# Optimization experiments

Hardware: AMD Instinct MI355X
Metric: run time of the kernel (lower is better)

Reference implementation:

```python
import jax, jax.numpy as jnp
from jax import lax
import numpy as np

B, N, C = 4, 2000, 80           # images, proposals/img, foreground classes
SCORE_THR = 0.05
IOU_THR = 0.5
MAX_PER_IMG = 100
K_PRE = 2000                     # pre-NMS top-k candidates per image
STDS = np.array([0.1, 0.1, 0.2, 0.2], dtype=np.float32)
MAX_RATIO = float(abs(np.log(16.0 / 1000.0)))  # wh_ratio_clip=16/1000


def setup_inputs() -> dict:
    key = jax.random.key(0)
    k1, k2, k3 = jax.random.split(key, 3)
    class_outs = jax.random.normal(k1, (B, N, C + 1), dtype=jnp.float32)
    regression_outs = jax.random.normal(k2, (B, N, C * 4), dtype=jnp.float32) * 0.5
    # random valid proposal boxes inside 800x1333 images (x1<x2, y1<y2)
    xy = jax.random.uniform(k3, (B, N, 2, 2), dtype=jnp.float32)
    xy = xy * jnp.array([1333.0, 800.0], dtype=jnp.float32)
    lo = jnp.min(xy, axis=2)
    hi = jnp.max(xy, axis=2) + 1.0
    boxes = jnp.concatenate([lo, hi], axis=-1)  # [B,N,4] x1,y1,x2,y2
    images_hw = jnp.tile(jnp.array([[800, 1333]], dtype=jnp.int32), (B, 1))
    return {"class_outs": class_outs, "regression_outs": regression_outs,
            "boxes": boxes, "images_hw": images_hw}


def _decode(props, deltas, h, w):
    # props [N,4], deltas [N,C,4] -> decoded boxes [N,C,4], clipped to image
    d = deltas * jnp.asarray(STDS)
    dx, dy, dw, dh = d[..., 0], d[..., 1], d[..., 2], d[..., 3]
    dw = jnp.clip(dw, -MAX_RATIO, MAX_RATIO)
    dh = jnp.clip(dh, -MAX_RATIO, MAX_RATIO)
    px = (props[:, None, 0] + props[:, None, 2]) * 0.5
    py = (props[:, None, 1] + props[:, None, 3]) * 0.5
    pw = props[:, None, 2] - props[:, None, 0]
    ph = props[:, None, 3] - props[:, None, 1]
    gx = px + pw * dx
    gy = py + ph * dy
    gw = pw * jnp.exp(dw)
    gh = ph * jnp.exp(dh)
    x1 = jnp.clip(gx - gw * 0.5, 0.0, w)
    y1 = jnp.clip(gy - gh * 0.5, 0.0, h)
    x2 = jnp.clip(gx + gw * 0.5, 0.0, w)
    y2 = jnp.clip(gy + gh * 0.5, 0.0, h)
    return jnp.stack([x1, y1, x2, y2], axis=-1)


def _pairwise_iou(b):
    # b [K,4] -> iou [K,K]
    area = (b[:, 2] - b[:, 0]) * (b[:, 3] - b[:, 1])
    lt = jnp.maximum(b[:, None, :2], b[None, :, :2])
    rb = jnp.minimum(b[:, None, 2:], b[None, :, 2:])
    wh = jnp.clip(rb - lt, 0.0)
    inter = wh[..., 0] * wh[..., 1]
    return inter / (area[:, None] + area[None, :] - inter + 1e-6)


def _process_image(cls_out, reg_out, props, hw):
    h = hw[0].astype(jnp.float32)
    w = hw[1].astype(jnp.float32)
    scores = jax.nn.softmax(cls_out, axis=-1)[:, :C]          # drop background col
    bboxes = _decode(props, reg_out.reshape(N, C, 4), h, w)   # [N,C,4]
    flat_scores = scores.reshape(-1)                          # [N*C]
    flat_boxes = bboxes.reshape(-1, 4)
    labels = jnp.tile(jnp.arange(C, dtype=jnp.int32), N)      # class fastest-varying
    cand = jnp.where(flat_scores > SCORE_THR, flat_scores, -1.0)
    top_scores, top_idx = lax.top_k(cand, K_PRE)
    top_boxes = flat_boxes[top_idx]
    top_labels = labels[top_idx]
    valid = top_scores > SCORE_THR
    # class-offset trick: boxes of distinct classes never overlap
    off = top_labels.astype(jnp.float32)[:, None] * (jnp.maximum(h, w) + 1.0)
    iou = _pairwise_iou(top_boxes + off)                      # [K_PRE,K_PRE]
    idxs = jnp.arange(K_PRE)

    def body(i, keep):
        sup = (idxs > i) & (iou[i] > IOU_THR) & keep[i]
        return keep & ~sup

    keep = lax.fori_loop(0, K_PRE, body, valid)
    kept_scores = jnp.where(keep, top_scores, -1.0)
    det_scores, det_i = lax.top_k(kept_scores, MAX_PER_IMG)
    det_valid = det_scores > SCORE_THR
    det_boxes = jnp.where(det_valid[:, None], top_boxes[det_i], 0.0)
    det_labels = jnp.where(det_valid, top_labels[det_i], -1)
    det_scores = jnp.where(det_valid, det_scores, 0.0)
    return det_boxes, det_scores, det_labels


def reference(class_outs, regression_outs, boxes, images_hw):
    det_boxes, det_scores, det_labels = jax.vmap(_process_image)(
        class_outs, regression_outs, boxes, images_hw)
    return det_boxes, det_scores, det_labels
```

## Files before the change

### kernel.cpp

```cpp
#include <hip/hip_runtime.h>


typedef unsigned long long u64;
typedef unsigned int u32;

#define B_ 4
#define N_ 2000
#define C_ 80
#define NCLS 81
#define KPRE 2000
#define MAXDET 100
#define TARGET 192
#define NB 2312
#define NBPAD 2368
#define NG 37
#define HBASE 0xF500
#define KSHIFT 46
#define CAPA 256
#define CAPB 2048
#define CAPIMG 8192
#define KPT 8
#define BPI 125
#define BIGI 0x7fffffff
#define MAXR 4.135166556742356f

#define WS_GCUR  0
#define WS_GHIST 64
#define WS_GFLAG 37952
#define WS_GKEYS 38016
#define WS_GBOX  300160
#define WS_ZEND  37952

__device__ __forceinline__ u64 pack_key(float score, unsigned fi) {
  return ((u64)__float_as_uint(score) << 32) | (u64)(0xFFFFFFFFu - fi);
}
__device__ __forceinline__ int bucket_of_bits(u32 sb) {
  return min(max((int)(sb >> 14) - HBASE, 0), NB - 1);
}
__device__ __forceinline__ u64 rdlane64(u64 v, int l) {
  u32 lo = (u32)__builtin_amdgcn_readlane((int)(u32)v, l);
  u32 hi = (u32)__builtin_amdgcn_readlane((int)(v >> 32), l);
  return ((u64)hi << 32) | lo;
}

__device__ __forceinline__ float wred_max(float v) {
  int t;
#define STEPM(ctrl)                                                          \
  t = __builtin_amdgcn_update_dpp(__float_as_int(v), __float_as_int(v),      \
                                  (ctrl), 0xF, 0xF, false);                  \
  v = fmaxf(v, __int_as_float(t));
  STEPM(0x111) STEPM(0x112) STEPM(0x114) STEPM(0x118) STEPM(0x142) STEPM(0x143)
#undef STEPM
  return __int_as_float(__builtin_amdgcn_readlane(__float_as_int(v), 63));
}
__device__ __forceinline__ float wred_sum(float v) {
  int t;
#define STEPS(ctrl)                                                          \
  t = __builtin_amdgcn_update_dpp(0, __float_as_int(v), (ctrl), 0xF, 0xF,    \
                                  false);                                    \
  v = v + __int_as_float(t);
  STEPS(0x111) STEPS(0x112) STEPS(0x114) STEPS(0x118) STEPS(0x142) STEPS(0x143)
#undef STEPS
  return __int_as_float(__builtin_amdgcn_readlane(__float_as_int(v), 63));
}

__device__ __forceinline__ float4 decode_one(
    u64 kk, const float* __restrict__ reg, const float* __restrict__ props,
    int b, float h, float w, float offscale) {
  unsigned fi = 0xFFFFFFFFu - (u32)kk;
  int n = (int)(fi / (unsigned)C_);
  int c = (int)(fi - (unsigned)n * (unsigned)C_);
  float4 p = ((const float4*)props)[b * N_ + n];
  const float* dl = reg + ((size_t)(b * N_ + n)) * (C_ * 4) + c * 4;
  float dx = dl[0] * 0.1f;
  float dy = dl[1] * 0.1f;
  float dw = fminf(fmaxf(dl[2] * 0.2f, -MAXR), MAXR);
  float dh = fminf(fmaxf(dl[3] * 0.2f, -MAXR), MAXR);
  float px = (p.x + p.z) * 0.5f, py = (p.y + p.w) * 0.5f;
  float pw = p.z - p.x, ph = p.w - p.y;
  float gx = px + pw * dx, gy = py + ph * dy;
  float gw = pw * expf(dw), gh = ph * expf(dh);
  float off = (float)c * offscale;
  return make_float4(fminf(fmaxf(gx - gw * 0.5f, 0.0f), w) + off,
                     fminf(fmaxf(gy - gh * 0.5f, 0.0f), h) + off,
                     fminf(fmaxf(gx + gw * 0.5f, 0.0f), w) + off,
                     fminf(fmaxf(gy + gh * 0.5f, 0.0f), h) + off);
}

__global__ __launch_bounds__(1024) void cand_kernel(
    const float* __restrict__ cls, const float* __restrict__ reg,
    const float* __restrict__ props, const int* __restrict__ hw,
    u64* __restrict__ gkeys, float4* __restrict__ gbox,
    u32* __restrict__ gcur, u32* __restrict__ ghist) {
  __shared__ int s_wc[16], s_woff[16];
  __shared__ int s_base;
  const int tid = threadIdx.x;
  const int wvi = tid >> 6, lane = tid & 63;
  const int blk = blockIdx.x;
  const int b = blk / BPI;
  const int n = (blk % BPI) * 16 + wvi;
  const float* lg = cls + (size_t)(b * N_ + n) * NCLS;
  float x0 = lg[lane];
  float x1 = (lane < 17) ? lg[64 + lane] : -3.0e38f;
  float mx = wred_max(fmaxf(x0, x1));
  float e0 = expf(x0 - mx);
  float e1 = (lane < 17) ? expf(x1 - mx) : 0.0f;
  float sum = wred_sum(e0 + e1);
  float sc0 = e0 / sum, sc1 = e1 / sum;
  bool p0 = sc0 > 0.05f;
  bool p1 = (lane < 16) && (sc1 > 0.05f);
  u64 m0 = __ballot(p0), m1 = __ballot(p1);
  int c0 = __popcll(m0);
  if (lane == 0) s_wc[wvi] = c0 + __popcll(m1);
  __syncthreads();
  if (tid == 0) {
    int acc = 0;
#pragma unroll
    for (int i = 0; i < 16; ++i) { s_woff[i] = acc; acc += s_wc[i]; }
    s_base = (acc > 0) ? (int)atomicAdd(&gcur[b], (u32)acc) : 0;
  }
  __syncthreads();
  const int base = s_base + s_woff[wvi];
  const u64 lt = (1ull << lane) - 1;
  u64* gk = gkeys + (size_t)b * CAPIMG;
  float4* gbx = gbox + (size_t)b * CAPIMG;
  u32* gh = ghist + (size_t)b * NBPAD;
  float hh = (float)hw[b * 2 + 0];
  float ww = (float)hw[b * 2 + 1];
  float offscale = fmaxf(hh, ww) + 1.0f;
  float4 p = ((const float4*)props)[b * N_ + n];
  float px = (p.x + p.z) * 0.5f, py = (p.y + p.w) * 0.5f;
  float pw = p.z - p.x, ph = p.w - p.y;
#pragma unroll 1
  for (int t = 0; t < 2; t++) {
    bool pp = t ? p1 : p0;
    if (!pp) continue;
    float sc = t ? sc1 : sc0;
    int c = t ? (64 + lane) : lane;
    int slot = base + (t ? (c0 + __popcll(m1 & lt)) : __popcll(m0 & lt));
    atomicAdd(&gh[bucket_of_bits(__float_as_uint(sc))], 1u);
    if (slot < CAPIMG) {
      gk[slot] = pack_key(sc, (unsigned)(n * C_ + c));
      const float4 d4 =
          *(const float4*)(reg + ((size_t)(b * N_ + n)) * (C_ * 4) + c * 4);
      float dx = d4.x * 0.1f, dy = d4.y * 0.1f;
      float dw = fminf(fmaxf(d4.z * 0.2f, -MAXR), MAXR);
      float dh = fminf(fmaxf(d4.w * 0.2f, -MAXR), MAXR);
      float gx = px + pw * dx, gy = py + ph * dy;
      float gw = pw * expf(dw), gh2 = ph * expf(dh);
      float off = (float)c * offscale;
      gbx[slot] = make_float4(fminf(fmaxf(gx - gw * 0.5f, 0.0f), ww) + off,
                              fminf(fmaxf(gy - gh2 * 0.5f, 0.0f), hh) + off,
                              fminf(fmaxf(gx + gw * 0.5f, 0.0f), ww) + off,
                              fminf(fmaxf(gy + gh2 * 0.5f, 0.0f), hh) + off);
    }
  }
}

__global__ __launch_bounds__(1024) void nms_kernel(
    const int* __restrict__ hw, const u64* __restrict__ gkeys,
    const float4* __restrict__ gbox, const u32* __restrict__ gcur,
    const u32* __restrict__ ghist, int* __restrict__ gflag,
    float* __restrict__ out) {
  __shared__ u64 lds8[3596];
  char* bp = (char*)lds8;
  u64* U = (u64*)bp;
  u64* SS = (u64*)(bp + 2080);
  u64* rb = (u64*)(bp + 4128);
  float4* bxA = (float4*)(bp + 12320);
  u32* s_hist = (u32*)(bp + 16416);
  u32* Upos = (u32*)(bp + 25888);
  int* rankA = (int*)(bp + 26912);
  int* outl = (int*)(bp + 27936);
  int* s_coarse = (int*)(bp + 28448);
  int* misc = (int*)(bp + 28704);

  const int b = blockIdx.x, tid = threadIdx.x;
  const int wv = tid >> 6, lane = tid & 63;

  if (tid < 16 && tid != 5 && tid != 7) misc[tid] = 0;
  if (tid >= NG && tid < 64) s_coarse[tid] = 0;
  if (tid == 512) {
    u32 Mraw = gcur[b];
    misc[5] = min((int)Mraw, CAPIMG);
    misc[7] = (Mraw > (u32)CAPIMG) ? 1 : 0;
  }

  for (int g2 = wv; g2 < NG; g2 += 16) {
    int v = (int)ghist[b * NBPAD + ((g2 << 6) | lane)];
    s_hist[(g2 << 6) | lane] = (u32)v;
#pragma unroll
    for (int o = 32; o; o >>= 1) v += __shfl_xor(v, o);
    if (lane == 0) s_coarse[g2] = v;
  }
  __syncthreads();

  if (tid < 64) {
    int v = s_coarse[lane];
#pragma unroll
    for (int off = 1; off < 64; off <<= 1) {
      int src = lane + off;
      int o = __shfl(v, src < 64 ? src : 63);
      if (src < 64) v += o;
    }
    int Mtot = __shfl(v, 0);
    u64 pm = __ballot(v >= TARGET);
    int T_A = 0, S_A;
    if (pm) {
      int gs = 63 - __builtin_clzll(pm);
      int beyond = __shfl(v, gs + 1);
      int fv = (int)s_hist[(gs << 6) | lane];
#pragma unroll
      for (int off = 1; off < 64; off <<= 1) {
        int src = lane + off;
        int o = __shfl(fv, src < 64 ? src : 63);
        if (src < 64) fv += o;
      }
      int cum = beyond + fv;
      u64 pm2 = __ballot(cum >= TARGET);
      int tr = 63 - __builtin_clzll(pm2);
      T_A = (gs << 6) + tr;
      S_A = __shfl(cum, tr);
    } else {
      S_A = Mtot;
    }
    if (lane == 0) { misc[0] = T_A; misc[2] = S_A; misc[3] = Mtot; }
  }
  __syncthreads();

  const int T_A = misc[0], S_A = misc[2], Mtot = misc[3], M = misc[5];
  if (S_A > CAPA || misc[7] != 0) {
    if (tid == 0) gflag[b] = 1;
    return;
  }

  {
    const u64 lt = (1ull << lane) - 1;
    const u64* keys = gkeys + (size_t)b * CAPIMG;
    u64 cur = keys[tid];
#pragma unroll 1
    for (int r = 0; r < KPT; r++) {
      u64 nxt = (r + 1 < KPT) ? keys[tid + ((r + 1) << 10)] : 0ULL;
      int idx = tid + (r << 10);
      bool pr = (idx < M) && (bucket_of_bits((u32)(cur >> 32)) >= T_A);
      u64 mk = __ballot(pr);
      if (mk) {
        int wbase = 0;
        if (lane == 0) wbase = atomicAdd(&misc[4], __popcll(mk));
        wbase = __shfl(wbase, 0);
        if (pr) {
          int pos = wbase + __popcll(mk & lt);
          if (pos < CAPA) { U[pos] = cur; Upos[pos] = (u32)idx; }
        }
      }
      cur = nxt;
    }
  }
  __syncthreads();
  int S = misc[4];
  if (S > CAPA) S = CAPA;
  if (tid == 0 && (S & 1)) U[S] = 0ULL;
  __syncthreads();

  if (tid < S) {
    u64 k1 = U[tid];
    int r1 = 0;
    const ulonglong2* Uu2 = (const ulonglong2*)U;
    int half = (S + 1) >> 1;
    for (int k = 0; k < half; k++) {
      ulonglong2 kk = Uu2[k];
      r1 += (kk.x > k1) + (kk.y > k1);
    }
    rankA[tid] = r1;
  }
  __syncthreads();
  if (tid < S) {
    int r1 = rankA[tid];
    SS[r1] = U[tid];
    bxA[r1] = gbox[(size_t)b * CAPIMG + Upos[tid]];
  }
  __syncthreads();

  int nwords = (S + 63) >> 6;
  int ntiles = nwords * (nwords + 1) / 2;
  for (int t = wv; t < ntiles; t += 16) {
    int ti = 0, rem = t;
    while (rem >= nwords - ti) { rem -= nwords - ti; ti++; }
    int tj = ti + rem;
    int i = (ti << 6) + lane;
    float4 bi4 = bxA[i];
    float ai = (bi4.z - bi4.x) * (bi4.w - bi4.y);
    u64 bits = 0;
    int jbase = tj << 6;
    int jcount = min(64, S - jbase);
    for (int jj = 0; jj < jcount; jj++) {
      int j = jbase + jj;
      float4 bj = bxA[j];
      float aj = (bj.z - bj.x) * (bj.w - bj.y);
      float iw = fmaxf(fminf(bi4.z, bj.z) - fmaxf(bi4.x, bj.x), 0.0f);
      float ih = fmaxf(fminf(bi4.w, bj.w) - fmaxf(bi4.y, bj.y), 0.0f);
      float inter = iw * ih;
      float iou = inter / (ai + aj - inter + 1e-6f);
      if (j > i && iou > 0.5f) bits |= (1ull << jj);
    }
    if (i < S) rb[i * 4 + tj] = bits;
  }
  __syncthreads();

  if (tid < 64) {
    u64 R[4][4];
#pragma unroll
    for (int c2 = 0; c2 < 4; c2++) {
#pragma unroll
      for (int w2 = 0; w2 < 4; w2++) {
        R[c2][w2] = (w2 >= c2) ? rb[((c2 << 6) + lane) * 4 + w2] : 0ull;
      }
    }
    u64 al[4];
#pragma unroll
    for (int w2 = 0; w2 < 4; w2++) {
      int lo = w2 << 6;
      al[w2] = (S > lo) ? ((S - lo >= 64) ? ~0ull : ((1ull << (S - lo)) - 1))
                        : 0ull;
    }
    int nk = 0;
#pragma unroll
    for (int c2 = 0; c2 < 4; c2++) {
      u64 a = al[c2];
      while (a) {
        int i = __builtin_ctzll(a);
        if (lane == 0) outl[nk] = (c2 << 6) + i;
        nk++;
        if (nk >= MAXDET) break;
        a &= a - 1;
        a &= ~rdlane64(R[c2][c2], i);
#pragma unroll
        for (int w2 = c2 + 1; w2 < 4; w2++)
          al[w2] &= ~rdlane64(R[c2][w2], i);
      }
      if (nk >= MAXDET) break;
    }
    if (lane == 0) misc[6] = nk;
  }
  __syncthreads();
  const int nkept = misc[6];
  bool modeB = (nkept < MAXDET && S < Mtot && S < KPRE);
  if (tid == 0) gflag[b] = modeB ? 1 : 0;
  if (modeB) return;

  float h = (float)hw[b * 2 + 0];
  float w = (float)hw[b * 2 + 1];
  float offscale = fmaxf(h, w) + 1.0f;
  float* oBox = out;
  float* oSc = out + B_ * MAXDET * 4;
  float* oLb = out + B_ * MAXDET * 5;
  if (tid < MAXDET) {
    float4 bb = make_float4(0.0f, 0.0f, 0.0f, 0.0f);
    float sv = 0.0f, lv = -1.0f;
    if (tid < nkept) {
      int idx = outl[tid];
      u64 kk = SS[idx];
      sv = __uint_as_float((u32)(kk >> 32));
      unsigned fi = 0xFFFFFFFFu - (u32)kk;
      int c = (int)(fi % (unsigned)C_);
      float off = (float)c * offscale;
      float4 ob = bxA[idx];
      bb = make_float4(ob.x - off, ob.y - off, ob.z - off, ob.w - off);
      lv = (float)c;
    }
    oBox[(b * MAXDET + tid) * 4 + 0] = bb.x;
    oBox[(b * MAXDET + tid) * 4 + 1] = bb.y;
    oBox[(b * MAXDET + tid) * 4 + 2] = bb.z;
    oBox[(b * MAXDET + tid) * 4 + 3] = bb.w;
    oSc[b * MAXDET + tid] = sv;
    oLb[b * MAXDET + tid] = lv;
  }
}

__global__ __launch_bounds__(1024) void nmsB_kernel(
    const float* __restrict__ reg, const float* __restrict__ props,
    const int* __restrict__ hw, const u64* __restrict__ gkeys,
    const u32* __restrict__ gcur, const int* __restrict__ gflag,
    float* __restrict__ out) {
  const int b = blockIdx.x, tid = threadIdx.x;
  if (gflag[b] == 0) return;

  __shared__ u64 lds8[7952];
  char* bp = (char*)lds8;
  u32* hist = (u32*)(bp + 0);
  u64* U2 = (u64*)(bp + 9472);
  u64* SSB = (u64*)(bp + 25856);
  int* outl = (int*)(bp + 42240);
  int* misc = (int*)(bp + 42752);
  const int lane = tid & 63;

  float h = (float)hw[b * 2 + 0];
  float w = (float)hw[b * 2 + 1];
  float offscale = fmaxf(h, w) + 1.0f;

  const u64* keys = gkeys + (size_t)b * CAPIMG;
  const int M = min((int)gcur[b], CAPIMG);

  for (int i = tid; i < NBPAD; i += 1024) hist[i] = 0;
  if (tid < 16) misc[tid] = 0;
  __syncthreads();

  for (int idx = tid; idx < M; idx += 1024) {
    u64 key = keys[idx];
    int bi = min(max((int)(key >> KSHIFT) - HBASE, 0), NB - 1);
    atomicAdd(&hist[bi], 1u);
  }
  __syncthreads();

  if (tid == 0) {
    int acc = 0, tb = 0;
    for (int bi = NB - 1; bi >= 0; bi--) {
      acc += (int)hist[bi];
      if (acc >= KPRE) { tb = bi; break; }
    }
    if (acc > CAPB) tb = min(tb + 1, NB - 1);
    misc[1] = tb;
    misc[4] = 0;
  }
  __syncthreads();
  int T_B = misc[1];

  for (int idx0 = 0; idx0 < M; idx0 += 1024) {
    int idx = idx0 + tid;
    bool pred = false;
    u64 key = 0;
    if (idx < M) {
      key = keys[idx];
      int bi = min(max((int)(key >> KSHIFT) - HBASE, 0), NB - 1);
      pred = (bi >= T_B);
    }
    u64 mk = __ballot(pred);
    if (mk) {
      int wbase = 0;
      if (lane == 0) wbase = atomicAdd(&misc[4], __popcll(mk));
      wbase = __shfl(wbase, 0);
      if (pred) {
        int pos = wbase + __popcll(mk & ((1ull << lane) - 1));
        if (pos < CAPB) U2[pos] = key;
      }
    }
  }
  __syncthreads();
  int S = misc[4];
  if (S > CAPB) S = CAPB;
  {
    int j1 = tid, j2 = tid + 1024;
    u64 k1 = (j1 < S) ? U2[j1] : 0ULL;
    u64 k2 = (j2 < S) ? U2[j2] : 0ULL;
    int r1 = 0, r2 = 0;
    for (int k = 0; k < S; k++) {
      u64 kk = U2[k];
      r1 += (kk > k1);
      r2 += (kk > k2);
    }
    __syncthreads();
    if (j1 < S) SSB[r1] = k1;
    if (j2 < S) SSB[r2] = k2;
  }
  __syncthreads();
  int K = (S < KPRE) ? S : KPRE;
  int j1 = tid, j2 = tid + 1024;
  bool kp1 = (j1 < K), kp2 = (j2 < K);
  float4 bb1 = kp1 ? decode_one(SSB[j1], reg, props, b, h, w, offscale)
                   : make_float4(0, 0, 0, 0);
  float4 bb2 = kp2 ? decode_one(SSB[j2], reg, props, b, h, w, offscale)
                   : make_float4(0, 0, 0, 0);
  int nk = 0;
  if (K > 0) {
    int i = 0;
    for (;;) {
      if (tid == 0) { outl[nk] = i; misc[5] = K; }
      nk++;
      if (nk >= MAXDET) break;
      __syncthreads();
      float4 tb = decode_one(SSB[i], reg, props, b, h, w, offscale);
      float ai = (tb.z - tb.x) * (tb.w - tb.y);
      int ln = K;
      if (kp1 && j1 > i) {
        float aj = (bb1.z - bb1.x) * (bb1.w - bb1.y);
        float iw = fmaxf(fminf(tb.z, bb1.z) - fmaxf(tb.x, bb1.x), 0.0f);
        float ih = fmaxf(fminf(tb.w, bb1.w) - fmaxf(tb.y, bb1.y), 0.0f);
        float inter = iw * ih;
        float iou = inter / (ai + aj - inter + 1e-6f);
        if (iou > 0.5f) kp1 = false;
        else ln = min(ln, j1);
      }
      if (kp2 && j2 > i) {
        float aj = (bb2.z - bb2.x) * (bb2.w - bb2.y);
        float iw = fmaxf(fminf(tb.z, bb2.z) - fmaxf(tb.x, bb2.x), 0.0f);
        float ih = fmaxf(fminf(tb.w, bb2.w) - fmaxf(tb.y, bb2.y), 0.0f);
        float inter = iw * ih;
        float iou = inter / (ai + aj - inter + 1e-6f);
        if (iou > 0.5f) kp2 = false;
        else ln = min(ln, j2);
      }
#pragma unroll
      for (int off = 32; off; off >>= 1) ln = min(ln, __shfl_xor(ln, off));
      if ((tid & 63) == 0 && ln < K) atomicMin(&misc[5], ln);
      __syncthreads();
      int ni = misc[5];
      __syncthreads();
      if (ni >= K) break;
      i = ni;
    }
  }
  if (tid == 0) misc[6] = nk;
  __syncthreads();
  int nkept = misc[6];

  float* oBox = out;
  float* oSc = out + B_ * MAXDET * 4;
  float* oLb = out + B_ * MAXDET * 5;
  for (int k2 = tid; k2 < MAXDET; k2 += 1024) {
    float4 bb = make_float4(0.0f, 0.0f, 0.0f, 0.0f);
    float sv = 0.0f, lv = -1.0f;
    if (k2 < nkept) {
      int idx = outl[k2];
      u64 kk = SSB[idx];
      sv = __uint_as_float((u32)(kk >> 32));
      unsigned fi = 0xFFFFFFFFu - (u32)kk;
      int c = (int)(fi % (unsigned)C_);
      float off = (float)c * offscale;
      float4 ob = decode_one(kk, reg, props, b, h, w, offscale);
      bb = make_float4(ob.x - off, ob.y - off, ob.z - off, ob.w - off);
      lv = (float)c;
    }
    oBox[(b * MAXDET + k2) * 4 + 0] = bb.x;
    oBox[(b * MAXDET + k2) * 4 + 1] = bb.y;
    oBox[(b * MAXDET + k2) * 4 + 2] = bb.z;
    oBox[(b * MAXDET + k2) * 4 + 3] = bb.w;
    oSc[b * MAXDET + k2] = sv;
    oLb[b * MAXDET + k2] = lv;
  }
}

extern "C" void kernel_launch(void* const* d_in, const int* in_sizes, int n_in,
                              void* d_out, int out_size, void* d_ws, size_t ws_size,
                              hipStream_t stream) {
  const float* cls = (const float*)d_in[0];
  const float* reg = (const float*)d_in[1];
  const float* props = (const float*)d_in[2];
  const int* hw = (const int*)d_in[3];
  float* out = (float*)d_out;

  u32* gcur = (u32*)((char*)d_ws + WS_GCUR);
  u32* ghist = (u32*)((char*)d_ws + WS_GHIST);
  int* gflag = (int*)((char*)d_ws + WS_GFLAG);
  u64* gkeys = (u64*)((char*)d_ws + WS_GKEYS);
  float4* gbox = (float4*)((char*)d_ws + WS_GBOX);

  hipMemsetAsync(d_ws, 0, WS_ZEND, stream);
  cand_kernel<<<B_ * BPI, 1024, 0, stream>>>(cls, reg, props, hw,
                                             gkeys, gbox, gcur, ghist);
  nms_kernel<<<B_, 1024, 0, stream>>>(hw, gkeys, gbox, gcur, ghist, gflag, out);
  nmsB_kernel<<<B_, 1024, 0, stream>>>(reg, props, hw, gkeys, gcur, gflag, out);
}
```

Before: 104.3 us.

## Compute histogram threshold in last cand block; shrink fast-path NMS candidate cap

The score-histogram threshold search moves out of the NMS kernel and into cand_kernel: the last block to finish for each image, detected through an atomic done counter, computes the threshold and writes it to the workspace. The NMS kernel now loads all of its keys into registers up front and reads the precomputed threshold. The fast-path candidate target and cap drop from 192/256 to 128/192, and the IoU bitmask tiles are split into 32-column halves so each wave handles one tile. This shortens the serial single-block NMS kernel, but more images may fall back to the slow modeB path, and it adds a cross-block atomic completion protocol.

```diff
diff --git a/kernel.cpp b/kernel.cpp
--- a/kernel.cpp
+++ b/kernel.cpp
@@ -10,13 +10,13 @@
 #define NCLS 81
 #define KPRE 2000
 #define MAXDET 100
-#define TARGET 192
+#define TARGET 128
 #define NB 2312
 #define NBPAD 2368
 #define NG 37
 #define HBASE 0xF500
 #define KSHIFT 46
-#define CAPA 256
+#define CAPA 192
 #define CAPB 2048
 #define CAPIMG 8192
 #define KPT 8
@@ -25,10 +25,12 @@
 #define MAXR 4.135166556742356f
 
 #define WS_GCUR  0
+#define WS_GDONE 16
 #define WS_GHIST 64
 #define WS_GFLAG 37952
-#define WS_GKEYS 38016
-#define WS_GBOX  300160
+#define WS_GTHR  37968
+#define WS_GKEYS 38080
+#define WS_GBOX  300224
 #define WS_ZEND  37952
 
 __device__ __forceinline__ u64 pack_key(float score, unsigned fi) {
@@ -91,7 +93,8 @@
     const float* __restrict__ cls, const float* __restrict__ reg,
     const float* __restrict__ props, const int* __restrict__ hw,
     u64* __restrict__ gkeys, float4* __restrict__ gbox,
-    u32* __restrict__ gcur, u32* __restrict__ ghist) {
+    u32* __restrict__ gcur, u32* __restrict__ gdone,
+    u32* __restrict__ ghist, int* __restrict__ gthr) {
   __shared__ int s_wc[16], s_woff[16];
   __shared__ int s_base;
   const int tid = threadIdx.x;
@@ -155,80 +158,87 @@
                               fminf(fmaxf(gy + gh2 * 0.5f, 0.0f), hh) + off);
     }
   }
+
+  __threadfence();
+  __syncthreads();
+  if (tid < 64) {
+    int done = 0;
+    if (lane == 0)
+      done = (int)__hip_atomic_fetch_add(&gdone[b], 1u, __ATOMIC_ACQ_REL,
+                                         __HIP_MEMORY_SCOPE_AGENT);
+    done = __shfl(done, 0);
+    if (done == BPI - 1) {
+      int acc = 0, T_A = 0, S_A = -1;
+      for (int g = NG - 1; g >= 0; --g) {
+        int v = (int)__hip_atomic_load(&gh[(g << 6) | lane], __ATOMIC_RELAXED,
+                                       __HIP_MEMORY_SCOPE_AGENT);
+        int gs = v;
+#pragma unroll
+        for (int o = 32; o; o >>= 1) gs += __shfl_xor(gs, o);
+        if (S_A < 0 && acc + gs >= TARGET) {
+          int fv = v;
+#pragma unroll
+          for (int off = 1; off < 64; off <<= 1) {
+            int src = lane + off;
+            int o = __shfl(fv, src < 64 ? src : 63);
+            if (src < 64) fv += o;
+          }
+          int cum = acc + fv;
+          u64 pm2 = __ballot(cum >= TARGET);
+          int tr = 63 - __builtin_clzll(pm2);
+          T_A = (g << 6) + tr;
+          S_A = __shfl(cum, tr);
+        }
+        acc += gs;
+      }
+      if (S_A < 0) { T_A = 0; S_A = acc; }
+      if (lane == 0) {
+        gthr[b * 4 + 0] = T_A;
+        gthr[b * 4 + 1] = S_A;
+        gthr[b * 4 + 2] = acc;
+      }
+    }
+  }
 }
 
 __global__ __launch_bounds__(1024) void nms_kernel(
     const int* __restrict__ hw, const u64* __restrict__ gkeys,
     const float4* __restrict__ gbox, const u32* __restrict__ gcur,
-    const u32* __restrict__ ghist, int* __restrict__ gflag,
+    const int* __restrict__ gthr, int* __restrict__ gflag,
     float* __restrict__ out) {
-  __shared__ u64 lds8[3596];
+  __shared__ u64 lds8[1802];
   char* bp = (char*)lds8;
   u64* U = (u64*)bp;
-  u64* SS = (u64*)(bp + 2080);
-  u64* rb = (u64*)(bp + 4128);
-  float4* bxA = (float4*)(bp + 12320);
-  u32* s_hist = (u32*)(bp + 16416);
-  u32* Upos = (u32*)(bp + 25888);
-  int* rankA = (int*)(bp + 26912);
-  int* outl = (int*)(bp + 27936);
-  int* s_coarse = (int*)(bp + 28448);
-  int* misc = (int*)(bp + 28704);
+  u64* SS = (u64*)(bp + 1552);
+  u64* rb = (u64*)(bp + 3088);
+  float4* bxA = (float4*)(bp + 9232);
+  u32* Upos = (u32*)(bp + 12304);
+  int* rankA = (int*)(bp + 13072);
+  int* outl = (int*)(bp + 13840);
+  int* misc = (int*)(bp + 14352);
 
   const int b = blockIdx.x, tid = threadIdx.x;
   const int wv = tid >> 6, lane = tid & 63;
 
-  if (tid < 16 && tid != 5 && tid != 7) misc[tid] = 0;
-  if (tid >= NG && tid < 64) s_coarse[tid] = 0;
+  const u64* keys = gkeys + (size_t)b * CAPIMG;
+  u64 kreg[KPT];
+#pragma unroll
+  for (int r = 0; r < KPT; r++) kreg[r] = keys[tid + (r << 10)];
+
+  if (tid == 0) misc[4] = 0;
+  if (tid == 64) {
+    misc[0] = gthr[b * 4 + 0];
+    misc[1] = gthr[b * 4 + 1];
+    misc[2] = gthr[b * 4 + 2];
+  }
   if (tid == 512) {
     u32 Mraw = gcur[b];
     misc[5] = min((int)Mraw, CAPIMG);
     misc[7] = (Mraw > (u32)CAPIMG) ? 1 : 0;
   }
-
-  for (int g2 = wv; g2 < NG; g2 += 16) {
-    int v = (int)ghist[b * NBPAD + ((g2 << 6) | lane)];
-    s_hist[(g2 << 6) | lane] = (u32)v;
-#pragma unroll
-    for (int o = 32; o; o >>= 1) v += __shfl_xor(v, o);
-    if (lane == 0) s_coarse[g2] = v;
-  }
-  __syncthreads();
-
-  if (tid < 64) {
-    int v = s_coarse[lane];
-#pragma unroll
-    for (int off = 1; off < 64; off <<= 1) {
-      int src = lane + off;
-      int o = __shfl(v, src < 64 ? src : 63);
-      if (src < 64) v += o;
-    }
-    int Mtot = __shfl(v, 0);
-    u64 pm = __ballot(v >= TARGET);
-    int T_A = 0, S_A;
-    if (pm) {
-      int gs = 63 - __builtin_clzll(pm);
-      int beyond = __shfl(v, gs + 1);
-      int fv = (int)s_hist[(gs << 6) | lane];
-#pragma unroll
-      for (int off = 1; off < 64; off <<= 1) {
-        int src = lane + off;
-        int o = __shfl(fv, src < 64 ? src : 63);
-        if (src < 64) fv += o;
-      }
-      int cum = beyond + fv;
-      u64 pm2 = __ballot(cum >= TARGET);
-      int tr = 63 - __builtin_clzll(pm2);
-      T_A = (gs << 6) + tr;
-      S_A = __shfl(cum, tr);
-    } else {
-      S_A = Mtot;
-    }
-    if (lane == 0) { misc[0] = T_A; misc[2] = S_A; misc[3] = Mtot; }
-  }
-  __syncthreads();
-
-  const int T_A = misc[0], S_A = misc[2], Mtot = misc[3], M = misc[5];
+  __syncthreads();
+
+  const int T_A = misc[0], S_A = misc[1], Mtot = misc[2], M = misc[5];
   if (S_A > CAPA || misc[7] != 0) {
     if (tid == 0) gflag[b] = 1;
     return;
@@ -236,13 +246,10 @@
 
   {
     const u64 lt = (1ull << lane) - 1;
-    const u64* keys = gkeys + (size_t)b * CAPIMG;
-    u64 cur = keys[tid];
 #pragma unroll 1
     for (int r = 0; r < KPT; r++) {
-      u64 nxt = (r + 1 < KPT) ? keys[tid + ((r + 1) << 10)] : 0ULL;
       int idx = tid + (r << 10);
-      bool pr = (idx < M) && (bucket_of_bits((u32)(cur >> 32)) >= T_A);
+      bool pr = (idx < M) && (bucket_of_bits((u32)(kreg[r] >> 32)) >= T_A);
       u64 mk = __ballot(pr);
       if (mk) {
         int wbase = 0;
@@ -250,10 +257,9 @@
         wbase = __shfl(wbase, 0);
         if (pr) {
           int pos = wbase + __popcll(mk & lt);
-          if (pos < CAPA) { U[pos] = cur; Upos[pos] = (u32)idx; }
+          if (pos < CAPA) { U[pos] = kreg[r]; Upos[pos] = (u32)idx; }
         }
       }
-      cur = nxt;
     }
   }
   __syncthreads();
@@ -282,50 +288,59 @@
   __syncthreads();
 
   int nwords = (S + 63) >> 6;
-  int ntiles = nwords * (nwords + 1) / 2;
-  for (int t = wv; t < ntiles; t += 16) {
-    int ti = 0, rem = t;
-    while (rem >= nwords - ti) { rem -= nwords - ti; ti++; }
-    int tj = ti + rem;
-    int i = (ti << 6) + lane;
-    float4 bi4 = bxA[i];
-    float ai = (bi4.z - bi4.x) * (bi4.w - bi4.y);
-    u64 bits = 0;
-    int jbase = tj << 6;
-    int jcount = min(64, S - jbase);
-    for (int jj = 0; jj < jcount; jj++) {
-      int j = jbase + jj;
-      float4 bj = bxA[j];
-      float aj = (bj.z - bj.x) * (bj.w - bj.y);
-      float iw = fmaxf(fminf(bi4.z, bj.z) - fmaxf(bi4.x, bj.x), 0.0f);
-      float ih = fmaxf(fminf(bi4.w, bj.w) - fmaxf(bi4.y, bj.y), 0.0f);
-      float inter = iw * ih;
-      float iou = inter / (ai + aj - inter + 1e-6f);
-      if (j > i && iou > 0.5f) bits |= (1ull << jj);
-    }
-    if (i < S) rb[i * 4 + tj] = bits;
+  int nh = (S + 31) >> 5;
+  {
+    int ti = 0, rem = wv;
+    bool have = false;
+    while (ti < nwords) {
+      int cnt = nh - 2 * ti;
+      if (cnt <= 0) break;
+      if (rem < cnt) { have = true; break; }
+      rem -= cnt;
+      ti++;
+    }
+    if (have) {
+      int tjh = 2 * ti + rem;
+      int i = (ti << 6) + lane;
+      float4 bi4 = bxA[i];
+      float ai = (bi4.z - bi4.x) * (bi4.w - bi4.y);
+      u32 bits = 0;
+      int jbase = tjh << 5;
+      int jcount = min(32, S - jbase);
+      for (int jj = 0; jj < jcount; jj++) {
+        int j = jbase + jj;
+        float4 bj = bxA[j];
+        float aj = (bj.z - bj.x) * (bj.w - bj.y);
+        float iw = fmaxf(fminf(bi4.z, bj.z) - fmaxf(bi4.x, bj.x), 0.0f);
+        float ih = fmaxf(fminf(bi4.w, bj.w) - fmaxf(bi4.y, bj.y), 0.0f);
+        float inter = iw * ih;
+        float iou = inter / (ai + aj - inter + 1e-6f);
+        if (j > i && iou > 0.5f) bits |= (1u << jj);
+      }
+      if (i < S) ((u32*)rb)[i * 8 + tjh] = bits;
+    }
   }
   __syncthreads();
 
   if (tid < 64) {
-    u64 R[4][4];
-#pragma unroll
-    for (int c2 = 0; c2 < 4; c2++) {
-#pragma unroll
-      for (int w2 = 0; w2 < 4; w2++) {
+    u64 R[3][3];
+#pragma unroll
+    for (int c2 = 0; c2 < 3; c2++) {
+#pragma unroll
+      for (int w2 = 0; w2 < 3; w2++) {
         R[c2][w2] = (w2 >= c2) ? rb[((c2 << 6) + lane) * 4 + w2] : 0ull;
       }
     }
-    u64 al[4];
-#pragma unroll
-    for (int w2 = 0; w2 < 4; w2++) {
+    u64 al[3];
+#pragma unroll
+    for (int w2 = 0; w2 < 3; w2++) {
       int lo = w2 << 6;
       al[w2] = (S > lo) ? ((S - lo >= 64) ? ~0ull : ((1ull << (S - lo)) - 1))
                         : 0ull;
     }
     int nk = 0;
 #pragma unroll
-    for (int c2 = 0; c2 < 4; c2++) {
+    for (int c2 = 0; c2 < 3; c2++) {
       u64 a = al[c2];
       while (a) {
         int i = __builtin_ctzll(a);
@@ -335,7 +350,7 @@
         a &= a - 1;
         a &= ~rdlane64(R[c2][c2], i);
 #pragma unroll
-        for (int w2 = c2 + 1; w2 < 4; w2++)
+        for (int w2 = c2 + 1; w2 < 3; w2++)
           al[w2] &= ~rdlane64(R[c2][w2], i);
       }
       if (nk >= MAXDET) break;
@@ -549,14 +564,16 @@
   float* out = (float*)d_out;
 
   u32* gcur = (u32*)((char*)d_ws + WS_GCUR);
+  u32* gdone = (u32*)((char*)d_ws + WS_GDONE);
   u32* ghist = (u32*)((char*)d_ws + WS_GHIST);
   int* gflag = (int*)((char*)d_ws + WS_GFLAG);
+  int* gthr = (int*)((char*)d_ws + WS_GTHR);
   u64* gkeys = (u64*)((char*)d_ws + WS_GKEYS);
   float4* gbox = (float4*)((char*)d_ws + WS_GBOX);
 
   hipMemsetAsync(d_ws, 0, WS_ZEND, stream);
-  cand_kernel<<<B_ * BPI, 1024, 0, stream>>>(cls, reg, props, hw,
-                                             gkeys, gbox, gcur, ghist);
-  nms_kernel<<<B_, 1024, 0, stream>>>(hw, gkeys, gbox, gcur, ghist, gflag, out);
+  cand_kernel<<<B_ * BPI, 1024, 0, stream>>>(cls, reg, props, hw, gkeys, gbox,
+                                             gcur, gdone, ghist, gthr);
+  nms_kernel<<<B_, 1024, 0, stream>>>(hw, gkeys, gbox, gcur, gthr, gflag, out);
   nmsB_kernel<<<B_, 1024, 0, stream>>>(reg, props, hw, gkeys, gcur, gflag, out);
 }
```

Result: slower. 257.6 us (+146.9%).

## Shrink fast-path candidate cap, prefetch keys early, split IoU tiles into half-words

Applied to the files above, without the earlier changes.

Lowers the histogram target and fast-path candidate capacity (256→192), which shrinks shared memory and the bitmask register array used in greedy NMS. All eight per-thread key loads are issued at kernel entry so their latency overlaps the histogram phase. The IoU mask tiles become 32-column half-words, one per wave, so the 16 waves share the triangular work more evenly without looping. The smaller cap risks sending more images to the slower fallback mode B when more than 192 candidates land above the threshold.

```diff
diff --git a/kernel.cpp b/kernel.cpp
--- a/kernel.cpp
+++ b/kernel.cpp
@@ -10,13 +10,13 @@
 #define NCLS 81
 #define KPRE 2000
 #define MAXDET 100
-#define TARGET 192
+#define TARGET 128
 #define NB 2312
 #define NBPAD 2368
 #define NG 37
 #define HBASE 0xF500
 #define KSHIFT 46
-#define CAPA 256
+#define CAPA 192
 #define CAPB 2048
 #define CAPIMG 8192
 #define KPT 8
@@ -162,21 +162,26 @@
     const float4* __restrict__ gbox, const u32* __restrict__ gcur,
     const u32* __restrict__ ghist, int* __restrict__ gflag,
     float* __restrict__ out) {
-  __shared__ u64 lds8[3596];
+  __shared__ u64 lds8[3018];
   char* bp = (char*)lds8;
   u64* U = (u64*)bp;
-  u64* SS = (u64*)(bp + 2080);
-  u64* rb = (u64*)(bp + 4128);
-  float4* bxA = (float4*)(bp + 12320);
-  u32* s_hist = (u32*)(bp + 16416);
-  u32* Upos = (u32*)(bp + 25888);
-  int* rankA = (int*)(bp + 26912);
-  int* outl = (int*)(bp + 27936);
-  int* s_coarse = (int*)(bp + 28448);
-  int* misc = (int*)(bp + 28704);
+  u64* SS = (u64*)(bp + 1552);
+  u64* rb = (u64*)(bp + 3088);
+  float4* bxA = (float4*)(bp + 9232);
+  u32* s_hist = (u32*)(bp + 12304);
+  u32* Upos = (u32*)(bp + 21776);
+  int* rankA = (int*)(bp + 22544);
+  int* outl = (int*)(bp + 23312);
+  int* s_coarse = (int*)(bp + 23824);
+  int* misc = (int*)(bp + 24080);
 
   const int b = blockIdx.x, tid = threadIdx.x;
   const int wv = tid >> 6, lane = tid & 63;
+
+  const u64* keys = gkeys + (size_t)b * CAPIMG;
+  u64 kreg[KPT];
+#pragma unroll
+  for (int r = 0; r < KPT; r++) kreg[r] = keys[tid + (r << 10)];
 
   if (tid < 16 && tid != 5 && tid != 7) misc[tid] = 0;
   if (tid >= NG && tid < 64) s_coarse[tid] = 0;
@@ -236,13 +241,10 @@
 
   {
     const u64 lt = (1ull << lane) - 1;
-    const u64* keys = gkeys + (size_t)b * CAPIMG;
-    u64 cur = keys[tid];
 #pragma unroll 1
     for (int r = 0; r < KPT; r++) {
-      u64 nxt = (r + 1 < KPT) ? keys[tid + ((r + 1) << 10)] : 0ULL;
       int idx = tid + (r << 10);
-      bool pr = (idx < M) && (bucket_of_bits((u32)(cur >> 32)) >= T_A);
+      bool pr = (idx < M) && (bucket_of_bits((u32)(kreg[r] >> 32)) >= T_A);
       u64 mk = __ballot(pr);
       if (mk) {
         int wbase = 0;
@@ -250,10 +252,9 @@
         wbase = __shfl(wbase, 0);
         if (pr) {
           int pos = wbase + __popcll(mk & lt);
-          if (pos < CAPA) { U[pos] = cur; Upos[pos] = (u32)idx; }
+          if (pos < CAPA) { U[pos] = kreg[r]; Upos[pos] = (u32)idx; }
         }
       }
-      cur = nxt;
     }
   }
   __syncthreads();
@@ -282,50 +283,59 @@
   __syncthreads();
 
   int nwords = (S + 63) >> 6;
-  int ntiles = nwords * (nwords + 1) / 2;
-  for (int t = wv; t < ntiles; t += 16) {
-    int ti = 0, rem = t;
-    while (rem >= nwords - ti) { rem -= nwords - ti; ti++; }
-    int tj = ti + rem;
-    int i = (ti << 6) + lane;
-    float4 bi4 = bxA[i];
-    float ai = (bi4.z - bi4.x) * (bi4.w - bi4.y);
-    u64 bits = 0;
-    int jbase = tj << 6;
-    int jcount = min(64, S - jbase);
-    for (int jj = 0; jj < jcount; jj++) {
-      int j = jbase + jj;
-      float4 bj = bxA[j];
-      float aj = (bj.z - bj.x) * (bj.w - bj.y);
-      float iw = fmaxf(fminf(bi4.z, bj.z) - fmaxf(bi4.x, bj.x), 0.0f);
-      float ih = fmaxf(fminf(bi4.w, bj.w) - fmaxf(bi4.y, bj.y), 0.0f);
-      float inter = iw * ih;
-      float iou = inter / (ai + aj - inter + 1e-6f);
-      if (j > i && iou > 0.5f) bits |= (1ull << jj);
-    }
-    if (i < S) rb[i * 4 + tj] = bits;
+  int nh = (S + 31) >> 5;
+  {
+    int ti = 0, rem = wv;
+    bool have = false;
+    while (ti < nwords) {
+      int cnt = nh - 2 * ti;
+      if (cnt <= 0) break;
+      if (rem < cnt) { have = true; break; }
+      rem -= cnt;
+      ti++;
+    }
+    if (have) {
+      int tjh = 2 * ti + rem;
+      int i = (ti << 6) + lane;
+      float4 bi4 = bxA[i];
+      float ai = (bi4.z - bi4.x) * (bi4.w - bi4.y);
+      u32 bits = 0;
+      int jbase = tjh << 5;
+      int jcount = min(32, S - jbase);
+      for (int jj = 0; jj < jcount; jj++) {
+        int j = jbase + jj;
+        float4 bj = bxA[j];
+        float aj = (bj.z - bj.x) * (bj.w - bj.y);
+        float iw = fmaxf(fminf(bi4.z, bj.z) - fmaxf(bi4.x, bj.x), 0.0f);
+        float ih = fmaxf(fminf(bi4.w, bj.w) - fmaxf(bi4.y, bj.y), 0.0f);
+        float inter = iw * ih;
+        float iou = inter / (ai + aj - inter + 1e-6f);
+        if (j > i && iou > 0.5f) bits |= (1u << jj);
+      }
+      if (i < S) ((u32*)rb)[i * 8 + tjh] = bits;
+    }
   }
   __syncthreads();
 
   if (tid < 64) {
-    u64 R[4][4];
-#pragma unroll
-    for (int c2 = 0; c2 < 4; c2++) {
-#pragma unroll
-      for (int w2 = 0; w2 < 4; w2++) {
+    u64 R[3][3];
+#pragma unroll
+    for (int c2 = 0; c2 < 3; c2++) {
+#pragma unroll
+      for (int w2 = 0; w2 < 3; w2++) {
         R[c2][w2] = (w2 >= c2) ? rb[((c2 << 6) + lane) * 4 + w2] : 0ull;
       }
     }
-    u64 al[4];
-#pragma unroll
-    for (int w2 = 0; w2 < 4; w2++) {
+    u64 al[3];
+#pragma unroll
+    for (int w2 = 0; w2 < 3; w2++) {
       int lo = w2 << 6;
       al[w2] = (S > lo) ? ((S - lo >= 64) ? ~0ull : ((1ull << (S - lo)) - 1))
                         : 0ull;
     }
     int nk = 0;
 #pragma unroll
-    for (int c2 = 0; c2 < 4; c2++) {
+    for (int c2 = 0; c2 < 3; c2++) {
       u64 a = al[c2];
       while (a) {
         int i = __builtin_ctzll(a);
@@ -335,7 +345,7 @@
         a &= a - 1;
         a &= ~rdlane64(R[c2][c2], i);
 #pragma unroll
-        for (int w2 = c2 + 1; w2 < 4; w2++)
+        for (int w2 = c2 + 1; w2 < 3; w2++)
           al[w2] &= ~rdlane64(R[c2][w2], i);
       }
       if (nk >= MAXDET) break;
```

Result: faster. 98.39 us (-5.7%).
